# Kernel tuning notes

Hardware: AMD Instinct MI355X
Metric: run time of the kernel (lower is better)

## Reference

```python
import jax, jax.numpy as jnp
import numpy as np

TAU = 2.0      # LIF membrane time constant
VTH = 1.0      # spike threshold
ALPHA = 2.0    # surrogate-gradient sharpness (atan surrogate)
EPS = 1e-5     # BatchNorm eps

@jax.custom_vjp
def spike(u):
    return (u > 0.0).astype(u.dtype)

def _spike_fwd(u):
    return spike(u), u

def _spike_bwd(u, g):
    sg = ALPHA / (2.0 * (1.0 + (jnp.pi / 2.0 * ALPHA * u) ** 2))
    return (g * sg,)

spike.defvjp(_spike_fwd, _spike_bwd)

def lif_time(x):
    # x: [B,T,C,H,W] -> spikes [B,T,C,H,W]; hard-reset LIF, v0 = 0
    xT = jnp.moveaxis(x, 1, 0)  # [T,B,C,H,W]
    def step(v, xt):
        v = v + (xt - v) / TAU
        s = spike(v - VTH)
        return v * (1.0 - s), s
    _, sT = jax.lax.scan(step, jnp.zeros_like(xT[0]), xT)
    return jnp.moveaxis(sT, 0, 1)

def conv2d(x, w, stride, pad):
    return jax.lax.conv_general_dilated(
        x, w, (stride, stride), [(pad, pad), (pad, pad)],
        dimension_numbers=('NCHW', 'OIHW', 'NCHW'))

def bn(x, gamma, beta, mean, var):
    # inference-style BatchNorm2d with running stats; x: [N,C,H,W]
    inv = gamma * jax.lax.rsqrt(var + EPS)
    return x * inv[None, :, None, None] + (beta - mean * inv)[None, :, None, None]

def setup_inputs() -> dict:
    key = jax.random.key(0)
    ks = jax.random.split(key, 16)
    B, T, Cin, Cout, H, W = 16, 8, 128, 256, 56, 56
    d = {}
    d['x_spike'] = (jax.random.uniform(ks[0], (B, T, Cin, H, W)) < 0.2).astype(jnp.float32)
    d['conv1_w'] = jax.random.normal(ks[1], (Cout, Cin, 3, 3), dtype=jnp.float32) * 0.05
    d['conv2_w'] = jax.random.normal(ks[2], (Cout, Cout, 3, 3), dtype=jnp.float32) * 0.05
    d['ds_w'] = jax.random.normal(ks[3], (Cout, Cin, 1, 1), dtype=jnp.float32) * 0.05
    for i, p in enumerate(['n1', 'n2', 'nd']):
        d[p + '_gamma'] = 1.0 + 0.1 * jax.random.normal(ks[4 + i], (Cout,), dtype=jnp.float32)
        d[p + '_beta'] = 0.1 * jax.random.normal(ks[7 + i], (Cout,), dtype=jnp.float32)
        d[p + '_mean'] = 0.01 * jax.random.normal(ks[10 + i], (Cout,), dtype=jnp.float32)
        d[p + '_var'] = jax.random.uniform(ks[13 + i], (Cout,), minval=0.5, maxval=1.5)
    return d

def reference(x_spike, conv1_w, conv2_w, ds_w,
              n1_gamma, n1_beta, n1_mean, n1_var,
              n2_gamma, n2_beta, n2_mean, n2_var,
              nd_gamma, nd_beta, nd_mean, nd_var):
    B, T, Cin, H, W = x_spike.shape
    x_flat = x_spike.reshape(B * T, Cin, H, W)
    # downsample shortcut (1x1 conv stride 2 + BN)
    identity = bn(conv2d(x_flat, ds_w, 2, 0), nd_gamma, nd_beta, nd_mean, nd_var)
    # NOTE: original module runs lif_shortcut on identity but DISCARDS the result
    # (pure state side-effect); it does not affect the output, so it is omitted.
    out = bn(conv2d(x_flat, conv1_w, 2, 1), n1_gamma, n1_beta, n1_mean, n1_var)
    Cout, Ho, Wo = out.shape[1], out.shape[2], out.shape[3]
    out = lif_time(out.reshape(B, T, Cout, Ho, Wo))
    out = bn(conv2d(out.reshape(B * T, Cout, Ho, Wo), conv2_w, 1, 1),
             n2_gamma, n2_beta, n2_mean, n2_var) + identity
    return lif_time(out.reshape(B, T, Cout, Ho, Wo))
```

## Files before the change

### kernel.cpp

```cpp
#include <hip/hip_runtime.h>
#include <hip/hip_bf16.h>

#define CIN  128
#define CO   256
#define HIN  56
#define WIN  56
#define OH   28
#define OWW  28
#define P    784
#define HWIN 3136
#define PERT 200704

typedef __attribute__((ext_vector_type(8))) short bf16x8v;
typedef __attribute__((ext_vector_type(4))) float f32x4;

__device__ __forceinline__ f32x4 mfma16(bf16x8v a, bf16x8v b, f32x4 c) {
    return __builtin_amdgcn_mfma_f32_16x16x32_bf16(a, b, c, 0, 0, 0);
}

__device__ __forceinline__ void gld_lds16(const void* g, void* l) {
    __builtin_amdgcn_global_load_lds(
        (const __attribute__((address_space(1))) void*)g,
        (__attribute__((address_space(3))) void*)l, 16, 0, 0);
}

__global__ __launch_bounds__(256) void k_prep_bias(
    const float* __restrict__ g1, const float* __restrict__ b1,
    const float* __restrict__ m1, const float* __restrict__ v1,
    const float* __restrict__ g2, const float* __restrict__ b2,
    const float* __restrict__ m2, const float* __restrict__ v2,
    const float* __restrict__ gd, const float* __restrict__ bd,
    const float* __restrict__ md, const float* __restrict__ vd,
    float* __restrict__ inv1o, float* __restrict__ bias1o,
    float* __restrict__ inv2o, float* __restrict__ invdo,
    float* __restrict__ bias2o)
{
    int co = threadIdx.x;
    float inv1 = g1[co] / sqrtf(v1[co] + 1e-5f);
    float inv2 = g2[co] / sqrtf(v2[co] + 1e-5f);
    float invd = gd[co] / sqrtf(vd[co] + 1e-5f);
    inv1o[co]  = inv1;
    bias1o[co] = fmaf(-m1[co], inv1, b1[co]);
    inv2o[co]  = inv2;
    invdo[co]  = invd;
    bias2o[co] = fmaf(-m2[co], inv2, b2[co]) + fmaf(-md[co], invd, bd[co]);
}

__global__ __launch_bounds__(256) void k_prep_w2p(
    const float* __restrict__ w2, const float* __restrict__ inv2,
    unsigned short* __restrict__ hi, unsigned short* __restrict__ lo)
{
    int i = blockIdx.x * 256 + threadIdx.x;
    if (i >= 73728) return;
    int tap = i >> 13;
    int r   = i & 8191;
    int ch  = r >> 10;
    int r2  = r & 1023;
    int cf  = r2 >> 6;
    int lane = r2 & 63;
    int co  = cf * 16 + (lane & 15);
    int cib = ch * 32 + (lane >> 4) * 8;
#pragma unroll
    for (int j = 0; j < 8; j++) {
        float w = w2[((size_t)co * CO + cib + j) * 9 + tap] * inv2[co];
        __hip_bfloat16 h = __float2bfloat16(w);
        __hip_bfloat16 l = __float2bfloat16(w - __bfloat162float(h));
        hi[(size_t)i * 8 + j] = *(unsigned short*)&h;
        lo[(size_t)i * 8 + j] = *(unsigned short*)&l;
    }
}

__global__ __launch_bounds__(256) void k_prep_w1p(
    const float* __restrict__ w1, const float* __restrict__ inv1,
    unsigned short* __restrict__ hi, unsigned short* __restrict__ mid,
    unsigned short* __restrict__ lo)
{
    int i = blockIdx.x * 256 + threadIdx.x;
    if (i >= 36864) return;
    int tap = i >> 12;
    int r   = i & 4095;
    int ch  = r >> 10;
    int r2  = r & 1023;
    int cf  = r2 >> 6;
    int lane = r2 & 63;
    int co  = cf * 16 + (lane & 15);
    int cib = ch * 32 + (lane >> 4) * 8;
#pragma unroll
    for (int j = 0; j < 8; j++) {
        float w = w1[((size_t)co * CIN + cib + j) * 9 + tap] * inv1[co];
        __hip_bfloat16 h = __float2bfloat16(w);
        float r1 = w - __bfloat162float(h);
        __hip_bfloat16 m = __float2bfloat16(r1);
        float r2f = r1 - __bfloat162float(m);
        __hip_bfloat16 l = __float2bfloat16(r2f);
        hi[(size_t)i * 8 + j]  = *(unsigned short*)&h;
        mid[(size_t)i * 8 + j] = *(unsigned short*)&m;
        lo[(size_t)i * 8 + j]  = *(unsigned short*)&l;
    }
}

__global__ __launch_bounds__(256) void k_prep_wdp(
    const float* __restrict__ wd, const float* __restrict__ invd,
    unsigned short* __restrict__ hi, unsigned short* __restrict__ lo)
{
    int i = blockIdx.x * 256 + threadIdx.x;
    if (i >= 4096) return;
    int ch  = i >> 10;
    int r2  = i & 1023;
    int cf  = r2 >> 6;
    int lane = r2 & 63;
    int co  = cf * 16 + (lane & 15);
    int cib = ch * 32 + (lane >> 4) * 8;
#pragma unroll
    for (int j = 0; j < 8; j++) {
        float w = wd[(size_t)co * CIN + cib + j] * invd[co];
        __hip_bfloat16 h = __float2bfloat16(w);
        __hip_bfloat16 l = __float2bfloat16(w - __bfloat162float(h));
        hi[(size_t)i * 8 + j] = *(unsigned short*)&h;
        lo[(size_t)i * 8 + j] = *(unsigned short*)&l;
    }
}

__global__ __launch_bounds__(256) void k_pack1(
    const float* __restrict__ x, unsigned int* __restrict__ xt_p)
{
    int i = blockIdx.x * 256 + threadIdx.x;
    int pos = i % HWIN;
    int nw  = i / HWIN;
    int w   = nw & 3;
    int n   = nw >> 2;
    const float* xp = x + ((size_t)n * CIN + w * 32) * HWIN + pos;
    unsigned int word = 0;
#pragma unroll
    for (int ci = 0; ci < 32; ci++)
        if (xp[(size_t)ci * HWIN] != 0.f) word |= (1u << ci);
    xt_p[((size_t)n * HWIN + pos) * 4 + w] = word;
}

__global__ __launch_bounds__(256) void k_conv1_mfma(
    const unsigned int* __restrict__ xt_p,
    const unsigned short* __restrict__ w1hip,
    const unsigned short* __restrict__ w1midp,
    const unsigned short* __restrict__ w1lop,
    const float* __restrict__ bias1,
    float* __restrict__ out)
{
    __shared__ unsigned int XW[4 * 522];

    const int n    = blockIdx.x / 7;
    const int rt   = blockIdx.x - n * 7;
    const int r0   = rt * 4;
    const int tid  = threadIdx.x;
    const int wave = tid >> 6;
    const int lane = tid & 63;
    const int l15  = lane & 15;
    const int quad = lane >> 4;
    const int cf0  = blockIdx.y * 8 + wave * 2;

    const unsigned int* xp_n = xt_p + (size_t)n * HWIN * 4;
    for (int i = tid; i < 513; i += 256) {
        int row = i / 57, c = i - row * 57;
        int irow = 2 * r0 - 1 + row;
        int iw   = c - 1;
        uint4 val = {0u, 0u, 0u, 0u};
        if (irow >= 0 && iw >= 0)
            val = *(const uint4*)(xp_n + (size_t)(irow * WIN + iw) * 4);
        int base = row * 58 + c;
        XW[0 * 522 + base] = val.x;
        XW[1 * 522 + base] = val.y;
        XW[2 * 522 + base] = val.z;
        XW[3 * 522 + base] = val.w;
    }
    __syncthreads();

    int rr[7], cc[7];
#pragma unroll
    for (int f = 0; f < 7; f++) {
        int pos = f * 16 + l15;
        rr[f] = pos / 28;
        cc[f] = pos - rr[f] * 28;
    }

    f32x4 acc[2][7];
#pragma unroll
    for (int g = 0; g < 2; g++)
#pragma unroll
        for (int f = 0; f < 7; f++) acc[g][f] = (f32x4){0.f, 0.f, 0.f, 0.f};

    bf16x8v ch0, cm0, cl0, ch1, cm1, cl1;
    bf16x8v nh0, nm0, nl0, nh1, nm1, nl1;
    {
        size_t b0 = ((size_t)(0 * 4 + 0) * 16 + cf0) * 512 + lane * 8;
        ch0 = *(const bf16x8v*)(w1hip + b0);  cm0 = *(const bf16x8v*)(w1midp + b0);
        cl0 = *(const bf16x8v*)(w1lop + b0);
        ch1 = *(const bf16x8v*)(w1hip + b0 + 512); cm1 = *(const bf16x8v*)(w1midp + b0 + 512);
        cl1 = *(const bf16x8v*)(w1lop + b0 + 512);
        nh0 = ch0; nm0 = cm0; nl0 = cl0; nh1 = ch1; nm1 = cm1; nl1 = cl1;
    }

    for (int c = 0; c < 4; c++) {
        for (int tap = 0; tap < 9; tap++) {
            int rd = c * 9 + tap;
            if (rd < 35) {
                int rn = rd + 1, cn = rn / 9, tn = rn - cn * 9;
                size_t b0 = ((size_t)(tn * 4 + cn) * 16 + cf0) * 512 + lane * 8;
                nh0 = *(const bf16x8v*)(w1hip + b0);  nm0 = *(const bf16x8v*)(w1midp + b0);
                nl0 = *(const bf16x8v*)(w1lop + b0);
                nh1 = *(const bf16x8v*)(w1hip + b0 + 512); nm1 = *(const bf16x8v*)(w1midp + b0 + 512);
                nl1 = *(const bf16x8v*)(w1lop + b0 + 512);
            }
            const int kh = tap / 3, kw = tap - kh * 3;
#pragma unroll
            for (int f = 0; f < 7; f++) {
                unsigned int word = XW[c * 522 + (2 * rr[f] + kh) * 58 + 2 * cc[f] + kw];
                unsigned int byt  = (word >> (quad * 8)) & 0xffu;
                uint4 u;
                u.x = ((byt & 1u)   ? 0x3F80u : 0u) | ((byt & 2u)   ? 0x3F800000u : 0u);
                u.y = ((byt & 4u)   ? 0x3F80u : 0u) | ((byt & 8u)   ? 0x3F800000u : 0u);
                u.z = ((byt & 16u)  ? 0x3F80u : 0u) | ((byt & 32u)  ? 0x3F800000u : 0u);
                u.w = ((byt & 64u)  ? 0x3F80u : 0u) | ((byt & 128u) ? 0x3F800000u : 0u);
                union { uint4 q; bf16x8v v; } cv;
                cv.q = u;
                acc[0][f] = mfma16(ch0, cv.v, acc[0][f]);
                acc[0][f] = mfma16(cm0, cv.v, acc[0][f]);
                acc[0][f] = mfma16(cl0, cv.v, acc[0][f]);
                acc[1][f] = mfma16(ch1, cv.v, acc[1][f]);
                acc[1][f] = mfma16(cm1, cv.v, acc[1][f]);
                acc[1][f] = mfma16(cl1, cv.v, acc[1][f]);
            }
            ch0 = nh0; cm0 = nm0; cl0 = nl0; ch1 = nh1; cm1 = nm1; cl1 = nl1;
        }
    }

#pragma unroll
    for (int g = 0; g < 2; g++)
#pragma unroll
        for (int f = 0; f < 7; f++) {
            int pg = rt * 112 + f * 16 + l15;
#pragma unroll
            for (int reg = 0; reg < 4; reg++) {
                int co = cf0 * 16 + g * 16 + quad * 4 + reg;
                out[((size_t)n * CO + co) * P + pg] = acc[g][f][reg] + bias1[co];
            }
        }
}

__global__ __launch_bounds__(256) void k_lif1t(
    const float* __restrict__ pre, unsigned short* __restrict__ st)
{
    __shared__ unsigned short T[16 * 68];
    const int b   = blockIdx.x;
    const int co0 = blockIdx.y * 64;
    const int p0  = blockIdx.z * 16;
    const int tid  = threadIdx.x;
    const int pcol = tid & 15;
    const int g    = tid >> 4;
    float v[4] = {0.f, 0.f, 0.f, 0.f};
    for (int t = 0; t < 8; t++) {
        const float* src = pre + (((size_t)(b * 8 + t)) * CO + co0) * P + p0;
        unsigned short s[4];
#pragma unroll
        for (int j = 0; j < 4; j++) {
            int co = g + 16 * j;
            float xv = src[(size_t)co * P + pcol];
            v[j] = v[j] + (xv - v[j]) * 0.5f;
            bool sp = v[j] > 1.0f;
            s[j] = sp ? 0x3F80 : 0;
            if (sp) v[j] = 0.f;
        }
        __syncthreads();
#pragma unroll
        for (int j = 0; j < 4; j++) T[pcol * 68 + g + 16 * j] = s[j];
        __syncthreads();
        int co  = co0 + pcol * 4;
        int chp = co >> 5, cio = co & 31;
        unsigned short* dst = st + (((size_t)(b * 8 + t) * 8 + chp) * P + (p0 + g)) * 32 + cio;
        ushort4 o;
        o.x = T[g * 68 + pcol * 4 + 0];
        o.y = T[g * 68 + pcol * 4 + 1];
        o.z = T[g * 68 + pcol * 4 + 2];
        o.w = T[g * 68 + pcol * 4 + 3];
        *(ushort4*)dst = o;
    }
}

__global__ __launch_bounds__(256) void k_conv2_mfma(
    const unsigned short* __restrict__ spike_t,
    const float* __restrict__ x,
    const unsigned short* __restrict__ w2hip,
    const unsigned short* __restrict__ w2lop,
    const unsigned short* __restrict__ wdhip,
    const unsigned short* __restrict__ wdlop,
    const float* __restrict__ bias2,
    float* __restrict__ out)
{
    __shared__ unsigned short SB[2 * 5760];

    const int n    = blockIdx.x / 7;
    const int rt   = blockIdx.x - n * 7;
    const int r0   = rt * 4;
    const int tid  = threadIdx.x;
    const int wave = tid >> 6;
    const int lane = tid & 63;
    const int l15  = lane & 15;
    const int quad = lane >> 4;
    const int cf0  = blockIdx.y * 8 + wave * 2;

    {
        uint4 z = {0u, 0u, 0u, 0u};
        for (int i = tid; i < 1440; i += 256) ((uint4*)SB)[i] = z;
    }
    __syncthreads();

    int  g_irow[3], g_lds[3];
    bool g_ok[3];
    int  g_half[3];
#pragma unroll
    for (int k = 0; k < 3; k++) {
        int idx  = wave * 3 + k;
        int row  = idx >> 1, half = idx & 1;
        int irow = r0 - 1 + row;
        g_irow[k] = irow;
        g_half[k] = half;
        g_ok[k]   = ((unsigned)irow < 28u) && (half == 0 || lane < 48);
        g_lds[k]  = row * 1920 + 64 + half * 1024;
    }
    const char* sp_n = (const char*)spike_t + (size_t)n * 8 * P * 64;

#pragma unroll
    for (int k = 0; k < 3; k++)
        if (g_ok[k])
            gld_lds16(sp_n + (size_t)g_irow[k] * 1792 + g_half[k] * 1024 + lane * 16,
                      (char*)SB + g_lds[k]);
    __syncthreads();

    int rr[7], cc[7];
#pragma unroll
    for (int f = 0; f < 7; f++) {
        int pos = f * 16 + l15;
        rr[f] = pos / 28;
        cc[f] = pos - rr[f] * 28;
    }

    f32x4 acc[2][7];
#pragma unroll
    for (int g = 0; g < 2; g++)
#pragma unroll
        for (int f = 0; f < 7; f++) acc[g][f] = (f32x4){0.f, 0.f, 0.f, 0.f};

    bf16x8v ch0, cl0, ch1, cl1, nh0, nl0, nh1, nl1;
    {
        size_t b0 = ((size_t)0 * 16 + cf0) * 512 + lane * 8;
        ch0 = *(const bf16x8v*)(w2hip + b0);
        cl0 = *(const bf16x8v*)(w2lop + b0);
        ch1 = *(const bf16x8v*)(w2hip + b0 + 512);
        cl1 = *(const bf16x8v*)(w2lop + b0 + 512);
        nh0 = ch0; nl0 = cl0; nh1 = ch1; nl1 = cl1;
    }

    for (int c = 0; c < 8; c++) {
        if (c < 7) {
            const char* base = sp_n + (size_t)(c + 1) * 50176;
            char* dstb = (char*)SB + ((c + 1) & 1) * 11520;
#pragma unroll
            for (int k = 0; k < 3; k++)
                if (g_ok[k])
                    gld_lds16(base + (size_t)g_irow[k] * 1792 + g_half[k] * 1024 + lane * 16,
                              dstb + g_lds[k]);
        }
        const int bufsh = (c & 1) * 5760;
        for (int tap = 0; tap < 9; tap++) {
            int rd = c * 9 + tap;
            if (rd < 71) {
                int rn = rd + 1, cn = rn / 9, tn = rn - cn * 9;
                size_t b0 = ((size_t)(tn * 8 + cn) * 16 + cf0) * 512 + lane * 8;
                nh0 = *(const bf16x8v*)(w2hip + b0);
                nl0 = *(const bf16x8v*)(w2lop + b0);
                nh1 = *(const bf16x8v*)(w2hip + b0 + 512);
                nl1 = *(const bf16x8v*)(w2lop + b0 + 512);
            }
            const int kh = tap / 3, kw = tap - kh * 3;
#pragma unroll
            for (int f = 0; f < 7; f++) {
                int slot = (rr[f] + kh) * 30 + cc[f] + kw;
                bf16x8v bfr = *(const bf16x8v*)(&SB[bufsh + slot * 32 + quad * 8]);
                acc[0][f] = mfma16(ch0, bfr, acc[0][f]);
                acc[0][f] = mfma16(cl0, bfr, acc[0][f]);
                acc[1][f] = mfma16(ch1, bfr, acc[1][f]);
                acc[1][f] = mfma16(cl1, bfr, acc[1][f]);
            }
            ch0 = nh0; cl0 = nl0; ch1 = nh1; cl1 = nl1;
        }
        __syncthreads();
    }

    const float* xb = x + (size_t)n * CIN * HWIN;
    for (int c = 0; c < 4; c++) {
        __syncthreads();
        for (int i = tid; i < 3584; i += 256) {
            int ci = i / 112, pos = i - ci * 112;
            int r = pos / 28, cl = pos - r * 28;
            float xv = xb[(size_t)(c * 32 + ci) * HWIN + (r0 + r) * 112 + cl * 2];
            __hip_bfloat16 h = __float2bfloat16(xv);
            SB[pos * 32 + ci] = *(unsigned short*)&h;
        }
        __syncthreads();
        size_t b0 = ((size_t)c * 16 + cf0) * 512 + lane * 8;
        bf16x8v a0h = *(const bf16x8v*)(wdhip + b0);
        bf16x8v a0l = *(const bf16x8v*)(wdlop + b0);
        bf16x8v a1h = *(const bf16x8v*)(wdhip + b0 + 512);
        bf16x8v a1l = *(const bf16x8v*)(wdlop + b0 + 512);
#pragma unroll
        for (int f = 0; f < 7; f++) {
            bf16x8v bfr = *(const bf16x8v*)(&SB[(f * 16 + l15) * 32 + quad * 8]);
            acc[0][f] = mfma16(a0h, bfr, acc[0][f]);
            acc[0][f] = mfma16(a0l, bfr, acc[0][f]);
            acc[1][f] = mfma16(a1h, bfr, acc[1][f]);
            acc[1][f] = mfma16(a1l, bfr, acc[1][f]);
        }
    }

#pragma unroll
    for (int g = 0; g < 2; g++)
#pragma unroll
        for (int f = 0; f < 7; f++) {
            int pg = rt * 112 + f * 16 + l15;
#pragma unroll
            for (int reg = 0; reg < 4; reg++) {
                int co = cf0 * 16 + g * 16 + quad * 4 + reg;
                out[((size_t)n * CO + co) * P + pg] = acc[g][f][reg] + bias2[co];
            }
        }
}

__global__ __launch_bounds__(256) void k_lif4(const float4* __restrict__ in,
                                              float4* __restrict__ out)
{
    const int q = PERT / 4;
    const int i = blockIdx.x * 256 + threadIdx.x;
    const int b = i / q;
    const int r = i - b * q;
    const float4* pi = in  + (size_t)(b * 8) * q + r;
    float4*       po = out + (size_t)(b * 8) * q + r;
    float v0 = 0.f, v1 = 0.f, v2 = 0.f, v3 = 0.f;
#pragma unroll
    for (int t = 0; t < 8; t++) {
        float4 xt = pi[(size_t)t * q];
        float4 s;
        v0 = v0 + (xt.x - v0) * 0.5f; s.x = (v0 > 1.0f) ? 1.f : 0.f; if (v0 > 1.0f) v0 = 0.f;
        v1 = v1 + (xt.y - v1) * 0.5f; s.y = (v1 > 1.0f) ? 1.f : 0.f; if (v1 > 1.0f) v1 = 0.f;
        v2 = v2 + (xt.z - v2) * 0.5f; s.z = (v2 > 1.0f) ? 1.f : 0.f; if (v2 > 1.0f) v2 = 0.f;
        v3 = v3 + (xt.w - v3) * 0.5f; s.w = (v3 > 1.0f) ? 1.f : 0.f; if (v3 > 1.0f) v3 = 0.f;
        po[(size_t)t * q] = s;
    }
}

extern "C" void kernel_launch(void* const* d_in, const int* in_sizes, int n_in,
                              void* d_out, int out_size, void* d_ws, size_t ws_size,
                              hipStream_t stream) {
    const float* x   = (const float*)d_in[0];
    const float* w1  = (const float*)d_in[1];
    const float* w2  = (const float*)d_in[2];
    const float* wd  = (const float*)d_in[3];
    const float* n1g = (const float*)d_in[4];
    const float* n1b = (const float*)d_in[5];
    const float* n1m = (const float*)d_in[6];
    const float* n1v = (const float*)d_in[7];
    const float* n2g = (const float*)d_in[8];
    const float* n2b = (const float*)d_in[9];
    const float* n2m = (const float*)d_in[10];
    const float* n2v = (const float*)d_in[11];
    const float* ndg = (const float*)d_in[12];
    const float* ndb = (const float*)d_in[13];
    const float* ndm = (const float*)d_in[14];
    const float* ndv = (const float*)d_in[15];

    float* out = (float*)d_out;

    char* w = (char*)d_ws;
    unsigned short* spike_t = (unsigned short*)w;
    unsigned short* w2hip   = (unsigned short*)(w + 51380224);
    unsigned short* w2lop   = (unsigned short*)(w + 52559872);
    unsigned short* w1hip   = (unsigned short*)(w + 53739520);
    unsigned short* w1midp  = (unsigned short*)(w + 54329344);
    unsigned short* w1lop   = (unsigned short*)(w + 54919168);
    unsigned short* wdhip   = (unsigned short*)(w + 55508992);
    unsigned short* wdlop   = (unsigned short*)(w + 55574528);
    float*          bias2   = (float*)(w + 55640064);
    float*          bias1   = (float*)(w + 55641088);
    float*          inv1    = (float*)(w + 55642112);
    float*          inv2    = (float*)(w + 55643136);
    float*          invd    = (float*)(w + 55644160);
    unsigned int*   xt_p    = (unsigned int*)(w + 55645184);

    k_prep_bias<<<1, 256, 0, stream>>>(n1g, n1b, n1m, n1v,
                                       n2g, n2b, n2m, n2v,
                                       ndg, ndb, ndm, ndv,
                                       inv1, bias1, inv2, invd, bias2);
    k_prep_w2p<<<288, 256, 0, stream>>>(w2, inv2, w2hip, w2lop);
    k_prep_w1p<<<144, 256, 0, stream>>>(w1, inv1, w1hip, w1midp, w1lop);
    k_prep_wdp<<<16, 256, 0, stream>>>(wd, invd, wdhip, wdlop);

    k_pack1<<<(128 * 4 * HWIN) / 256, 256, 0, stream>>>(x, xt_p);
    k_conv1_mfma<<<dim3(896, 2), 256, 0, stream>>>(
        xt_p, w1hip, w1midp, w1lop, bias1, out);
    k_lif1t<<<dim3(16, 4, 49), 256, 0, stream>>>(out, spike_t);
    k_conv2_mfma<<<dim3(896, 2), 256, 0, stream>>>(
        spike_t, x, w2hip, w2lop, wdhip, wdlop, bias2, out);
    k_lif4<<<(16 * (PERT / 4)) / 256, 256, 0, stream>>>(
        (const float4*)out, (float4*)out);
}
```

Before: 832.8 us.

## Swizzle spike tile layout for conflict-free LDS reads and reuse packed bitmask for downsample

New measurement: 875.9 us. 1.05x slower.

```diff
diff --git a/kernel.cpp b/kernel.cpp
--- a/kernel.cpp
+++ b/kernel.cpp
@@ -190,7 +190,7 @@
     bf16x8v ch0, cm0, cl0, ch1, cm1, cl1;
     bf16x8v nh0, nm0, nl0, nh1, nm1, nl1;
     {
-        size_t b0 = ((size_t)(0 * 4 + 0) * 16 + cf0) * 512 + lane * 8;
+        size_t b0 = ((size_t)0 * 16 + cf0) * 512 + lane * 8;
         ch0 = *(const bf16x8v*)(w1hip + b0);  cm0 = *(const bf16x8v*)(w1midp + b0);
         cl0 = *(const bf16x8v*)(w1lop + b0);
         ch1 = *(const bf16x8v*)(w1hip + b0 + 512); cm1 = *(const bf16x8v*)(w1midp + b0 + 512);
@@ -255,6 +255,13 @@
     const int tid  = threadIdx.x;
     const int pcol = tid & 15;
     const int g    = tid >> 4;
+    const int pos = p0 + g;
+    const int oh  = pos / 28, ow = pos - oh * 28;
+    const int f8  = ((((oh + 1) * 30 + ow + 1) >> 1) & 3);
+    const int o      = (pcol & 7) >> 1;
+    const int no     = o ^ f8;
+    const int within = (pcol & 1) * 4;
+    const int chp    = (co0 >> 5) + (pcol >> 3);
     float v[4] = {0.f, 0.f, 0.f, 0.f};
     for (int t = 0; t < 8; t++) {
         const float* src = pre + (((size_t)(b * 8 + t)) * CO + co0) * P + p0;
@@ -272,21 +279,20 @@
 #pragma unroll
         for (int j = 0; j < 4; j++) T[pcol * 68 + g + 16 * j] = s[j];
         __syncthreads();
-        int co  = co0 + pcol * 4;
-        int chp = co >> 5, cio = co & 31;
-        unsigned short* dst = st + (((size_t)(b * 8 + t) * 8 + chp) * P + (p0 + g)) * 32 + cio;
-        ushort4 o;
-        o.x = T[g * 68 + pcol * 4 + 0];
-        o.y = T[g * 68 + pcol * 4 + 1];
-        o.z = T[g * 68 + pcol * 4 + 2];
-        o.w = T[g * 68 + pcol * 4 + 3];
-        *(ushort4*)dst = o;
+        unsigned short* dst = st + (((size_t)(b * 8 + t) * 8 + chp) * P + pos) * 32
+                               + no * 8 + within;
+        ushort4 ov;
+        ov.x = T[g * 68 + pcol * 4 + 0];
+        ov.y = T[g * 68 + pcol * 4 + 1];
+        ov.z = T[g * 68 + pcol * 4 + 2];
+        ov.w = T[g * 68 + pcol * 4 + 3];
+        *(ushort4*)dst = ov;
     }
 }
 
 __global__ __launch_bounds__(256) void k_conv2_mfma(
     const unsigned short* __restrict__ spike_t,
-    const float* __restrict__ x,
+    const unsigned int* __restrict__ xt_p,
     const unsigned short* __restrict__ w2hip,
     const unsigned short* __restrict__ w2lop,
     const unsigned short* __restrict__ wdhip,
@@ -295,6 +301,7 @@
     float* __restrict__ out)
 {
     __shared__ unsigned short SB[2 * 5760];
+    __shared__ unsigned int   XW2[4 * 112];
 
     const int n    = blockIdx.x / 7;
     const int rt   = blockIdx.x - n * 7;
@@ -309,6 +316,15 @@
     {
         uint4 z = {0u, 0u, 0u, 0u};
         for (int i = tid; i < 1440; i += 256) ((uint4*)SB)[i] = z;
+    }
+    for (int i = tid; i < 112; i += 256) {
+        int r = i / 28, c = i - r * 28;
+        uint4 w4 = *(const uint4*)(xt_p + ((size_t)n * HWIN
+                    + (2 * (r0 + r)) * WIN + 2 * c) * 4);
+        XW2[0 * 112 + i] = w4.x;
+        XW2[1 * 112 + i] = w4.y;
+        XW2[2 * 112 + i] = w4.z;
+        XW2[3 * 112 + i] = w4.w;
     }
     __syncthreads();
 
@@ -383,7 +399,9 @@
 #pragma unroll
             for (int f = 0; f < 7; f++) {
                 int slot = (rr[f] + kh) * 30 + cc[f] + kw;
-                bf16x8v bfr = *(const bf16x8v*)(&SB[bufsh + slot * 32 + quad * 8]);
+                int sw   = (slot >> 1) & 3;
+                bf16x8v bfr = *(const bf16x8v*)(
+                    &SB[bufsh + slot * 32 + ((quad ^ sw) * 8)]);
                 acc[0][f] = mfma16(ch0, bfr, acc[0][f]);
                 acc[0][f] = mfma16(cl0, bfr, acc[0][f]);
                 acc[1][f] = mfma16(ch1, bfr, acc[1][f]);
@@ -394,17 +412,7 @@
         __syncthreads();
     }
 
-    const float* xb = x + (size_t)n * CIN * HWIN;
     for (int c = 0; c < 4; c++) {
-        __syncthreads();
-        for (int i = tid; i < 3584; i += 256) {
-            int ci = i / 112, pos = i - ci * 112;
-            int r = pos / 28, cl = pos - r * 28;
-            float xv = xb[(size_t)(c * 32 + ci) * HWIN + (r0 + r) * 112 + cl * 2];
-            __hip_bfloat16 h = __float2bfloat16(xv);
-            SB[pos * 32 + ci] = *(unsigned short*)&h;
-        }
-        __syncthreads();
         size_t b0 = ((size_t)c * 16 + cf0) * 512 + lane * 8;
         bf16x8v a0h = *(const bf16x8v*)(wdhip + b0);
         bf16x8v a0l = *(const bf16x8v*)(wdlop + b0);
@@ -412,11 +420,19 @@
         bf16x8v a1l = *(const bf16x8v*)(wdlop + b0 + 512);
 #pragma unroll
         for (int f = 0; f < 7; f++) {
-            bf16x8v bfr = *(const bf16x8v*)(&SB[(f * 16 + l15) * 32 + quad * 8]);
-            acc[0][f] = mfma16(a0h, bfr, acc[0][f]);
-            acc[0][f] = mfma16(a0l, bfr, acc[0][f]);
-            acc[1][f] = mfma16(a1h, bfr, acc[1][f]);
-            acc[1][f] = mfma16(a1l, bfr, acc[1][f]);
+            unsigned int word = XW2[c * 112 + rr[f] * 28 + cc[f]];
+            unsigned int byt  = (word >> (quad * 8)) & 0xffu;
+            uint4 u;
+            u.x = ((byt & 1u)   ? 0x3F80u : 0u) | ((byt & 2u)   ? 0x3F800000u : 0u);
+            u.y = ((byt & 4u)   ? 0x3F80u : 0u) | ((byt & 8u)   ? 0x3F800000u : 0u);
+            u.z = ((byt & 16u)  ? 0x3F80u : 0u) | ((byt & 32u)  ? 0x3F800000u : 0u);
+            u.w = ((byt & 64u)  ? 0x3F80u : 0u) | ((byt & 128u) ? 0x3F800000u : 0u);
+            union { uint4 q; bf16x8v v; } cv;
+            cv.q = u;
+            acc[0][f] = mfma16(a0h, cv.v, acc[0][f]);
+            acc[0][f] = mfma16(a0l, cv.v, acc[0][f]);
+            acc[1][f] = mfma16(a1h, cv.v, acc[1][f]);
+            acc[1][f] = mfma16(a1l, cv.v, acc[1][f]);
         }
     }
 
@@ -506,7 +522,7 @@
         xt_p, w1hip, w1midp, w1lop, bias1, out);
     k_lif1t<<<dim3(16, 4, 49), 256, 0, stream>>>(out, spike_t);
     k_conv2_mfma<<<dim3(896, 2), 256, 0, stream>>>(
-        spike_t, x, w2hip, w2lop, wdhip, wdlop, bias2, out);
+        spike_t, xt_p, w2hip, w2lop, wdhip, wdlop, bias2, out);
     k_lif4<<<(16 * (PERT / 4)) / 256, 256, 0, stream>>>(
         (const float4*)out, (float4*)out);
 }
```
